# Performance work log

Measured on AMD Instinct MI355X. Metric: run time of the kernel, lower is better.

The kernel has to match this reference:

```python
import jax, jax.numpy as jnp
import numpy as np

N = 4096       # number of graph nodes
F_IN = 512     # in_features == out_features (residual connection requires it)
H = 8          # n_heads


def setup_inputs() -> dict:
    key = jax.random.key(0)
    k1, k2, k3, k4, k5 = jax.random.split(key, 5)
    s = 1.0 / np.sqrt(F_IN)  # keep projections well-scaled
    x = jax.random.normal(k1, (N, F_IN), dtype=jnp.float32)
    Wq = jax.random.normal(k2, (F_IN, F_IN), dtype=jnp.float32) * s
    Wk = jax.random.normal(k3, (F_IN, F_IN), dtype=jnp.float32) * s
    Wv = jax.random.normal(k4, (F_IN, F_IN), dtype=jnp.float32) * s
    adj = jax.random.randint(k5, (H, N, N), 0, 2, dtype=jnp.int32)
    return {"x": x, "Wq": Wq, "Wk": Wk, "Wv": Wv, "adj": adj}


def reference(x, Wq, Wk, Wv, adj):
    # Faithful to torch GraphAttentionLayer.forward (eval mode, dropout off).
    # NOTE: the torch code builds keys = input.repeat(N,1,1).detach() -> the
    # K/V inputs are stop-gradient copies of x; projections are per-node, so
    # we compute them once instead of materializing the redundant [N,N,F].
    n, f = x.shape
    d = f // H  # head dim (chunk_size)
    xk = jax.lax.stop_gradient(x)
    # nn.Linear: y = x @ W.T ; split feature dim into heads -> [H, N, d]
    Q = (x @ Wq.T).reshape(n, H, d).transpose(1, 0, 2)
    K = (xk @ Wk.T).reshape(n, H, d).transpose(1, 0, 2)
    V = (xk @ Wv.T).reshape(n, H, d).transpose(1, 0, 2)
    # scaled by sqrt(in_features) (NOT head dim), as in the original
    scores = jnp.einsum('hnd,hmd->hnm', Q, K) / jnp.sqrt(jnp.float32(f))
    scores = jnp.where(adj > 0, scores, jnp.float32(-9e15))
    attn = jax.nn.softmax(scores, axis=-1)          # [H, N, N]
    out = jnp.einsum('hnm,hmd->hnd', attn, V)       # [H, N, d]
    out = out.transpose(1, 0, 2).reshape(n, f)      # concat heads -> [N, F]
    return jax.nn.elu(out + x)[:, None, :]          # [N, 1, F] like torch
```

## Files before the change

### kernel.cpp

```cpp
#include <hip/hip_runtime.h>
#include <hip/hip_bf16.h>

#define NN 4096
#define FF 512
#define NH 8
#define DH 64

typedef __attribute__((ext_vector_type(8))) short bf16x8;
typedef __attribute__((ext_vector_type(4))) float f32x4;

#define X_OFF  0
#define W_OFF  2097152
#define QF_OFF 2883584
#define KF_OFF 4980736
#define VF_OFF 7077888
#define PACC_OFF 9175040
#define PDEN_USHORT_OFF 17563648
#define PK_USHORT_OFF 17825792

__device__ __forceinline__ ushort f2bf(float f) {
    __hip_bfloat16 h = __float2bfloat16(f);
    return __builtin_bit_cast(ushort, h);
}
__device__ __forceinline__ float bf2f(ushort u) {
    unsigned int v = ((unsigned int)u) << 16;
    return __builtin_bit_cast(float, v);
}

__global__ __launch_bounds__(256) void cvt_kernel(const float* __restrict__ x,
                                                  const float* __restrict__ wq,
                                                  const float* __restrict__ wk,
                                                  const float* __restrict__ wv,
                                                  ushort* __restrict__ ws) {
    int i = blockIdx.x * 256 + threadIdx.x;
    int base = i * 4;
    const float* src;
    int off;
    float sc = 1.f;
    if (base < 2097152) { src = x; off = base; }
    else {
        int t = base - 2097152;
        int m = t >> 18;
        src = (m == 0) ? wq : ((m == 1) ? wk : wv);
        if (m == 0) sc = 0.044194173824159216f;
        off = t & 262143;
    }
    float4 v = *reinterpret_cast<const float4*>(src + off);
    ushort4 o;
    o.x = f2bf(v.x * sc); o.y = f2bf(v.y * sc); o.z = f2bf(v.z * sc); o.w = f2bf(v.w * sc);
    *reinterpret_cast<ushort4*>(ws + base) = o;
}

__global__ __launch_bounds__(256) void packqkv_kernel(const int* __restrict__ adj,
                                                      unsigned int* __restrict__ pk,
                                                      ushort* __restrict__ ws) {
    int bid = blockIdx.x;
    int wave = threadIdx.x >> 6, lane = threadIdx.x & 63;

    if (bid < 8192) {
        int row = bid * 4 + wave;
        const int* ar = adj + (size_t)row * 4096;
        unsigned long long* outp = reinterpret_cast<unsigned long long*>(pk + (size_t)row * 128);
        for (int it = 0; it < 64; it += 4) {
            int v0 = __builtin_nontemporal_load(ar + (it + 0) * 64 + lane);
            int v1 = __builtin_nontemporal_load(ar + (it + 1) * 64 + lane);
            int v2 = __builtin_nontemporal_load(ar + (it + 2) * 64 + lane);
            int v3 = __builtin_nontemporal_load(ar + (it + 3) * 64 + lane);
            unsigned long long b0 = __ballot(v0 != 0);
            unsigned long long b1 = __ballot(v1 != 0);
            unsigned long long b2 = __ballot(v2 != 0);
            unsigned long long b3 = __ballot(v3 != 0);
            if (lane == 0) {
                outp[it + 0] = b0;
                outp[it + 1] = b1;
                outp[it + 2] = b2;
                outp[it + 3] = b3;
            }
        }
        return;
    }

    int q = bid - 8192;
    int mat = q >> 9;
    int rem = q & 511;
    int fb = rem & 7;
    int mb = rem >> 3;
    int la = lane & 15, lk = lane >> 4;

    int m_base = mb * 64 + wave * 16;
    int f_base = fb * 64;

    const ushort* xb = ws + X_OFF;
    const ushort* wb = ws + W_OFF + mat * 262144;

    f32x4 acc[4];
#pragma unroll
    for (int t = 0; t < 4; ++t) acc[t] = (f32x4){0.f, 0.f, 0.f, 0.f};

#pragma unroll 4
    for (int k0 = 0; k0 < 512; k0 += 32) {
        bf16x8 a = *reinterpret_cast<const bf16x8*>(xb + (size_t)(m_base + la) * 512 + k0 + lk * 8);
#pragma unroll
        for (int ft = 0; ft < 4; ++ft) {
            bf16x8 b = *reinterpret_cast<const bf16x8*>(wb + (size_t)(f_base + ft * 16 + la) * 512 + k0 + lk * 8);
            acc[ft] = __builtin_amdgcn_mfma_f32_16x16x32_bf16(a, b, acc[ft], 0, 0, 0);
        }
    }

#pragma unroll
    for (int ft = 0; ft < 4; ++ft) {
#pragma unroll
        for (int r = 0; r < 4; ++r) {
            int n = m_base + lk * 4 + r;
            int d = ft * 16 + la;
            ushort v = f2bf(acc[ft][r]);
            if (mat < 2) {
                ushort* base = ws + (mat == 0 ? QF_OFF : KF_OFF) + (size_t)fb * 262144;
                int blk = n >> 4, rr = n & 15;
                int half = d >> 5, lkk = (d >> 3) & 3, e = d & 7;
                base[(((size_t)blk * 2 + half) * 64 + lkk * 16 + rr) * 8 + e] = v;
            } else {
                ushort* base = ws + VF_OFF + (size_t)fb * 262144;
                int kb64 = n >> 6, kc = n & 63;
                int hf = kc >> 5, lkv = (kc >> 3) & 3, ev = kc & 7;
                int dt = d >> 4, lav = d & 15;
                base[((((size_t)kb64 * 4 + dt) * 2 + hf) * 64 + lkv * 16 + lav) * 8 + ev] = v;
            }
        }
    }
}

__global__ __launch_bounds__(256, 3) void attn_kernel(const unsigned int* __restrict__ pk,
                                                      const ushort* __restrict__ ws,
                                                      ushort* __restrict__ pacc,
                                                      float* __restrict__ pden) {
    __shared__ ushort kbuf[2][8][512];
    __shared__ ushort vbuf[2][8][512];
    __shared__ ushort P[4][16][72];

    int bid = blockIdx.x;
    int h = bid & 7, qb = (bid >> 3) & 63, ks = bid >> 9;
    int wave = threadIdx.x >> 6, lane = threadIdx.x & 63;
    int la = lane & 15, lk = lane >> 4;
    int q0w = qb * 64 + wave * 16;
    int lk4 = lk * 4;

    const ushort* Qh = ws + QF_OFF + (size_t)h * 262144;
    const ushort* Kh = ws + KF_OFF + (size_t)h * 262144;
    const ushort* Vh = ws + VF_OFF + (size_t)h * 262144;
    const unsigned int* mrow = pk + ((size_t)h * 4096 + q0w + la) * 128;

    bf16x8 qa0 = *reinterpret_cast<const bf16x8*>(Qh + ((((size_t)(q0w >> 4)) * 2 + 0) * 64 + lane) * 8);
    bf16x8 qa1 = *reinterpret_cast<const bf16x8*>(Qh + ((((size_t)(q0w >> 4)) * 2 + 1) * 64 + lane) * 8);

    f32x4 acc[4];
#pragma unroll
    for (int r = 0; r < 4; ++r) acc[r] = (f32x4){0.f, 0.f, 0.f, 0.f};
    float den = 0.f;

    const f32x4 zero = {0.f, 0.f, 0.f, 0.f};
    int kb0 = ks * 16;

#define STAGE(BUF, KB)                                                                     \
    {                                                                                      \
        const ushort* sbase_ = (wave < 2) ? Kh : Vh;                                       \
        ushort(*dbuf_)[512] = (wave < 2) ? kbuf[BUF] : vbuf[BUF];                          \
        int t0_ = (wave & 1) * 4;                                                          \
        _Pragma("unroll")                                                                  \
        for (int t_ = 0; t_ < 4; ++t_) {                                                   \
            int tile_ = t0_ + t_;                                                          \
            const ushort* src_ = sbase_ +                                                  \
                (((size_t)(KB) * 4 + (tile_ >> 1)) * 2 + (tile_ & 1)) * 512 + lane * 8;    \
            __builtin_amdgcn_global_load_lds(                                              \
                (const __attribute__((address_space(1))) unsigned int*)src_,               \
                (__attribute__((address_space(3))) unsigned int*)&dbuf_[tile_][0],         \
                16, 0, 0);                                                                 \
        }                                                                                  \
    }

    STAGE(0, kb0)

    for (int it = 0; it < 16; ++it) {
        int kb = kb0 + it;
        int cur = it & 1;

        asm volatile("s_waitcnt vmcnt(0)" ::: "memory");
        __builtin_amdgcn_s_barrier();

        if (it < 15) STAGE(cur ^ 1, kb + 1)

        uint2 mk = *reinterpret_cast<const uint2*>(mrow + kb * 2);

#pragma unroll
        for (int kt = 0; kt < 4; ++kt) {
            bf16x8 kf0 = *reinterpret_cast<const bf16x8*>(&kbuf[cur][kt * 2 + 0][lane * 8]);
            bf16x8 kf1 = *reinterpret_cast<const bf16x8*>(&kbuf[cur][kt * 2 + 1][lane * 8]);
            f32x4 s = __builtin_amdgcn_mfma_f32_16x16x32_bf16(kf0, qa0, zero, 0, 0, 0);
            s = __builtin_amdgcn_mfma_f32_16x16x32_bf16(kf1, qa1, s, 0, 0, 0);
            unsigned int dw = (kt < 2) ? mk.x : mk.y;
            int sh = ((kt & 1) << 4) + lk4;
            ushort4 pw;
            float e0 = __expf(((dw >> (sh + 0)) & 1u) ? s[0] : -1e30f);
            float e1 = __expf(((dw >> (sh + 1)) & 1u) ? s[1] : -1e30f);
            float e2 = __expf(((dw >> (sh + 2)) & 1u) ? s[2] : -1e30f);
            float e3 = __expf(((dw >> (sh + 3)) & 1u) ? s[3] : -1e30f);
            den += (e0 + e1) + (e2 + e3);
            pw.x = f2bf(e0); pw.y = f2bf(e1); pw.z = f2bf(e2); pw.w = f2bf(e3);
            *reinterpret_cast<ushort4*>(&P[wave][la][kt * 16 + lk4]) = pw;
        }

        bf16x8 pa0 = *reinterpret_cast<const bf16x8*>(&P[wave][la][lk * 8]);
        bf16x8 pa1 = *reinterpret_cast<const bf16x8*>(&P[wave][la][32 + lk * 8]);
#pragma unroll
        for (int dt = 0; dt < 4; ++dt) {
            bf16x8 vb0 = *reinterpret_cast<const bf16x8*>(&vbuf[cur][dt * 2 + 0][lane * 8]);
            bf16x8 vb1 = *reinterpret_cast<const bf16x8*>(&vbuf[cur][dt * 2 + 1][lane * 8]);
            acc[dt] = __builtin_amdgcn_mfma_f32_16x16x32_bf16(pa0, vb0, acc[dt], 0, 0, 0);
            acc[dt] = __builtin_amdgcn_mfma_f32_16x16x32_bf16(pa1, vb1, acc[dt], 0, 0, 0);
        }
    }

    den += __shfl_xor(den, 16, 64);
    den += __shfl_xor(den, 32, 64);

    ushort* pa_out = pacc + ((size_t)ks * 8 + h) * 4096 * 64;
#pragma unroll
    for (int dt = 0; dt < 4; ++dt)
#pragma unroll
        for (int r = 0; r < 4; ++r) {
            int qi = q0w + lk4 + r;
            __builtin_nontemporal_store(f2bf(acc[dt][r]), pa_out + (size_t)qi * 64 + dt * 16 + la);
        }
    if (lane < 16) {
        float* pd = pden + ((size_t)ks * 8 + h) * 4096;
        pd[q0w + lane] = den;
    }
#undef STAGE
}

__global__ __launch_bounds__(256) void combine_kernel(const float* __restrict__ x,
                                                      const ushort* __restrict__ pacc,
                                                      const float* __restrict__ pden,
                                                      float* __restrict__ out) {
    int idx = blockIdx.x * 256 + threadIdx.x;
    int n = idx >> 7, fq = idx & 127;
    int h = fq >> 4;
    int d4 = (fq & 15) * 4;

    float4 o = make_float4(0.f, 0.f, 0.f, 0.f);
    float den = 0.f;
#pragma unroll
    for (int ksp = 0; ksp < 4; ++ksp) {
        const ushort* pa = pacc + (((size_t)ksp * 8 + h) * 4096 + n) * 64 + d4;
        ushort4 p = *reinterpret_cast<const ushort4*>(pa);
        o.x += bf2f(p.x); o.y += bf2f(p.y); o.z += bf2f(p.z); o.w += bf2f(p.w);
        den += pden[((size_t)ksp * 8 + h) * 4096 + n];
    }
    float4 xv = *reinterpret_cast<const float4*>(x + (size_t)n * 512 + fq * 4);
    float inv = 1.f / den;
    float4 r;
    r.x = o.x * inv + xv.x;
    r.y = o.y * inv + xv.y;
    r.z = o.z * inv + xv.z;
    r.w = o.w * inv + xv.w;
    r.x = (r.x > 0.f) ? r.x : (__expf(r.x) - 1.f);
    r.y = (r.y > 0.f) ? r.y : (__expf(r.y) - 1.f);
    r.z = (r.z > 0.f) ? r.z : (__expf(r.z) - 1.f);
    r.w = (r.w > 0.f) ? r.w : (__expf(r.w) - 1.f);
    *reinterpret_cast<float4*>(out + (size_t)n * 512 + fq * 4) = r;
}

extern "C" void kernel_launch(void* const* d_in, const int* in_sizes, int n_in,
                              void* d_out, int out_size, void* d_ws, size_t ws_size,
                              hipStream_t stream) {
    const float* x  = (const float*)d_in[0];
    const float* wq = (const float*)d_in[1];
    const float* wk = (const float*)d_in[2];
    const float* wv = (const float*)d_in[3];
    const int*   adj = (const int*)d_in[4];
    float* out = (float*)d_out;
    ushort* ws = (ushort*)d_ws;
    ushort* pacc = ws + PACC_OFF;
    float* pden = (float*)(ws + PDEN_USHORT_OFF);
    unsigned int* pk = (unsigned int*)(ws + PK_USHORT_OFF);

    cvt_kernel<<<2816, 256, 0, stream>>>(x, wq, wk, wv, ws);
    packqkv_kernel<<<9728, 256, 0, stream>>>(adj, pk, ws);
    attn_kernel<<<2048, 256, 0, stream>>>(pk, ws, pacc, pden);
    combine_kernel<<<2048, 256, 0, stream>>>(x, pacc, pden, out);
}
```

Baseline: 226.8 us.

## Process two query tiles per wave and split keys three ways

Each wave now handles 32 query rows instead of 16, so every K/V tile staged in LDS is reused across twice as many queries. The key dimension is split into 3 uneven chunks (22/21/21 blocks) instead of 4, which cuts the grid to 768 blocks and the partial-sum traffic read by the combine kernel. The aim is less LDS staging and global K/V traffic per unit of work. In exchange, register pressure rises and far fewer blocks are in flight, which may reduce occupancy and latency hiding on the GPU.

```diff
diff --git a/kernel.cpp b/kernel.cpp
--- a/kernel.cpp
+++ b/kernel.cpp
@@ -136,30 +136,39 @@
                                                       float* __restrict__ pden) {
     __shared__ ushort kbuf[2][8][512];
     __shared__ ushort vbuf[2][8][512];
-    __shared__ ushort P[4][16][72];
+    __shared__ ushort P[4][2][16][72];
 
     int bid = blockIdx.x;
-    int h = bid & 7, qb = (bid >> 3) & 63, ks = bid >> 9;
+    int h = bid & 7, qb = (bid >> 3) & 31, ks = bid >> 8;
     int wave = threadIdx.x >> 6, lane = threadIdx.x & 63;
     int la = lane & 15, lk = lane >> 4;
-    int q0w = qb * 64 + wave * 16;
+    int q0w = qb * 128 + wave * 32;
     int lk4 = lk * 4;
 
     const ushort* Qh = ws + QF_OFF + (size_t)h * 262144;
     const ushort* Kh = ws + KF_OFF + (size_t)h * 262144;
     const ushort* Vh = ws + VF_OFF + (size_t)h * 262144;
-    const unsigned int* mrow = pk + ((size_t)h * 4096 + q0w + la) * 128;
-
-    bf16x8 qa0 = *reinterpret_cast<const bf16x8*>(Qh + ((((size_t)(q0w >> 4)) * 2 + 0) * 64 + lane) * 8);
-    bf16x8 qa1 = *reinterpret_cast<const bf16x8*>(Qh + ((((size_t)(q0w >> 4)) * 2 + 1) * 64 + lane) * 8);
-
-    f32x4 acc[4];
-#pragma unroll
-    for (int r = 0; r < 4; ++r) acc[r] = (f32x4){0.f, 0.f, 0.f, 0.f};
-    float den = 0.f;
+    const unsigned int* mrow0 = pk + ((size_t)h * 4096 + q0w + la) * 128;
+    const unsigned int* mrow1 = mrow0 + 16 * 128;
+
+    bf16x8 qa[2][2];
+#pragma unroll
+    for (int qs = 0; qs < 2; ++qs)
+#pragma unroll
+        for (int hf = 0; hf < 2; ++hf)
+            qa[qs][hf] = *reinterpret_cast<const bf16x8*>(
+                Qh + ((((size_t)((q0w >> 4) + qs)) * 2 + hf) * 64 + lane) * 8);
+
+    f32x4 acc[2][4];
+    float den[2] = {0.f, 0.f};
+#pragma unroll
+    for (int qs = 0; qs < 2; ++qs)
+#pragma unroll
+        for (int r = 0; r < 4; ++r) acc[qs][r] = (f32x4){0.f, 0.f, 0.f, 0.f};
 
     const f32x4 zero = {0.f, 0.f, 0.f, 0.f};
-    int kb0 = ks * 16;
+    int kb_begin = ks * 21 + (ks ? 1 : 0);
+    int kb_count = 22 - (ks ? 1 : 0);
 
 #define STAGE(BUF, KB)                                                                     \
     {                                                                                      \
@@ -178,62 +187,78 @@
         }                                                                                  \
     }
 
-    STAGE(0, kb0)
-
-    for (int it = 0; it < 16; ++it) {
-        int kb = kb0 + it;
+    STAGE(0, kb_begin)
+
+    for (int it = 0; it < kb_count; ++it) {
+        int kb = kb_begin + it;
         int cur = it & 1;
 
         asm volatile("s_waitcnt vmcnt(0)" ::: "memory");
         __builtin_amdgcn_s_barrier();
 
-        if (it < 15) STAGE(cur ^ 1, kb + 1)
-
-        uint2 mk = *reinterpret_cast<const uint2*>(mrow + kb * 2);
+        if (it + 1 < kb_count) STAGE(cur ^ 1, kb + 1)
+
+        uint2 mk0 = *reinterpret_cast<const uint2*>(mrow0 + kb * 2);
+        uint2 mk1 = *reinterpret_cast<const uint2*>(mrow1 + kb * 2);
 
 #pragma unroll
         for (int kt = 0; kt < 4; ++kt) {
             bf16x8 kf0 = *reinterpret_cast<const bf16x8*>(&kbuf[cur][kt * 2 + 0][lane * 8]);
             bf16x8 kf1 = *reinterpret_cast<const bf16x8*>(&kbuf[cur][kt * 2 + 1][lane * 8]);
-            f32x4 s = __builtin_amdgcn_mfma_f32_16x16x32_bf16(kf0, qa0, zero, 0, 0, 0);
-            s = __builtin_amdgcn_mfma_f32_16x16x32_bf16(kf1, qa1, s, 0, 0, 0);
-            unsigned int dw = (kt < 2) ? mk.x : mk.y;
             int sh = ((kt & 1) << 4) + lk4;
-            ushort4 pw;
-            float e0 = __expf(((dw >> (sh + 0)) & 1u) ? s[0] : -1e30f);
-            float e1 = __expf(((dw >> (sh + 1)) & 1u) ? s[1] : -1e30f);
-            float e2 = __expf(((dw >> (sh + 2)) & 1u) ? s[2] : -1e30f);
-            float e3 = __expf(((dw >> (sh + 3)) & 1u) ? s[3] : -1e30f);
-            den += (e0 + e1) + (e2 + e3);
-            pw.x = f2bf(e0); pw.y = f2bf(e1); pw.z = f2bf(e2); pw.w = f2bf(e3);
-            *reinterpret_cast<ushort4*>(&P[wave][la][kt * 16 + lk4]) = pw;
-        }
-
-        bf16x8 pa0 = *reinterpret_cast<const bf16x8*>(&P[wave][la][lk * 8]);
-        bf16x8 pa1 = *reinterpret_cast<const bf16x8*>(&P[wave][la][32 + lk * 8]);
+#pragma unroll
+            for (int qs = 0; qs < 2; ++qs) {
+                f32x4 s = __builtin_amdgcn_mfma_f32_16x16x32_bf16(kf0, qa[qs][0], zero, 0, 0, 0);
+                s = __builtin_amdgcn_mfma_f32_16x16x32_bf16(kf1, qa[qs][1], s, 0, 0, 0);
+                unsigned int dw = qs ? ((kt < 2) ? mk1.x : mk1.y) : ((kt < 2) ? mk0.x : mk0.y);
+                ushort4 pw;
+                float e0 = __expf(((dw >> (sh + 0)) & 1u) ? s[0] : -1e30f);
+                float e1 = __expf(((dw >> (sh + 1)) & 1u) ? s[1] : -1e30f);
+                float e2 = __expf(((dw >> (sh + 2)) & 1u) ? s[2] : -1e30f);
+                float e3 = __expf(((dw >> (sh + 3)) & 1u) ? s[3] : -1e30f);
+                den[qs] += (e0 + e1) + (e2 + e3);
+                pw.x = f2bf(e0); pw.y = f2bf(e1); pw.z = f2bf(e2); pw.w = f2bf(e3);
+                *reinterpret_cast<ushort4*>(&P[wave][qs][la][kt * 16 + lk4]) = pw;
+            }
+        }
+
+        bf16x8 pa[2][2];
+#pragma unroll
+        for (int qs = 0; qs < 2; ++qs) {
+            pa[qs][0] = *reinterpret_cast<const bf16x8*>(&P[wave][qs][la][lk * 8]);
+            pa[qs][1] = *reinterpret_cast<const bf16x8*>(&P[wave][qs][la][32 + lk * 8]);
+        }
 #pragma unroll
         for (int dt = 0; dt < 4; ++dt) {
             bf16x8 vb0 = *reinterpret_cast<const bf16x8*>(&vbuf[cur][dt * 2 + 0][lane * 8]);
             bf16x8 vb1 = *reinterpret_cast<const bf16x8*>(&vbuf[cur][dt * 2 + 1][lane * 8]);
-            acc[dt] = __builtin_amdgcn_mfma_f32_16x16x32_bf16(pa0, vb0, acc[dt], 0, 0, 0);
-            acc[dt] = __builtin_amdgcn_mfma_f32_16x16x32_bf16(pa1, vb1, acc[dt], 0, 0, 0);
-        }
-    }
-
-    den += __shfl_xor(den, 16, 64);
-    den += __shfl_xor(den, 32, 64);
+            acc[0][dt] = __builtin_amdgcn_mfma_f32_16x16x32_bf16(pa[0][0], vb0, acc[0][dt], 0, 0, 0);
+            acc[0][dt] = __builtin_amdgcn_mfma_f32_16x16x32_bf16(pa[0][1], vb1, acc[0][dt], 0, 0, 0);
+            acc[1][dt] = __builtin_amdgcn_mfma_f32_16x16x32_bf16(pa[1][0], vb0, acc[1][dt], 0, 0, 0);
+            acc[1][dt] = __builtin_amdgcn_mfma_f32_16x16x32_bf16(pa[1][1], vb1, acc[1][dt], 0, 0, 0);
+        }
+    }
+
+#pragma unroll
+    for (int qs = 0; qs < 2; ++qs) {
+        den[qs] += __shfl_xor(den[qs], 16, 64);
+        den[qs] += __shfl_xor(den[qs], 32, 64);
+    }
 
     ushort* pa_out = pacc + ((size_t)ks * 8 + h) * 4096 * 64;
 #pragma unroll
-    for (int dt = 0; dt < 4; ++dt)
-#pragma unroll
-        for (int r = 0; r < 4; ++r) {
-            int qi = q0w + lk4 + r;
-            __builtin_nontemporal_store(f2bf(acc[dt][r]), pa_out + (size_t)qi * 64 + dt * 16 + la);
-        }
+    for (int qs = 0; qs < 2; ++qs)
+#pragma unroll
+        for (int dt = 0; dt < 4; ++dt)
+#pragma unroll
+            for (int r = 0; r < 4; ++r) {
+                int qi = q0w + qs * 16 + lk4 + r;
+                __builtin_nontemporal_store(f2bf(acc[qs][dt][r]), pa_out + (size_t)qi * 64 + dt * 16 + la);
+            }
     if (lane < 16) {
         float* pd = pden + ((size_t)ks * 8 + h) * 4096;
-        pd[q0w + lane] = den;
+        pd[q0w + lane] = den[0];
+        pd[q0w + 16 + lane] = den[1];
     }
 #undef STAGE
 }
@@ -250,7 +275,7 @@
     float4 o = make_float4(0.f, 0.f, 0.f, 0.f);
     float den = 0.f;
 #pragma unroll
-    for (int ksp = 0; ksp < 4; ++ksp) {
+    for (int ksp = 0; ksp < 3; ++ksp) {
         const ushort* pa = pacc + (((size_t)ksp * 8 + h) * 4096 + n) * 64 + d4;
         ushort4 p = *reinterpret_cast<const ushort4*>(pa);
         o.x += bf2f(p.x); o.y += bf2f(p.y); o.z += bf2f(p.z); o.w += bf2f(p.w);
@@ -286,6 +311,6 @@
 
     cvt_kernel<<<2816, 256, 0, stream>>>(x, wq, wk, wv, ws);
     packqkv_kernel<<<9728, 256, 0, stream>>>(adj, pk, ws);
-    attn_kernel<<<2048, 256, 0, stream>>>(pk, ws, pacc, pden);
+    attn_kernel<<<768, 256, 0, stream>>>(pk, ws, pacc, pden);
     combine_kernel<<<2048, 256, 0, stream>>>(x, pacc, pden, out);
 }
```

New measurement: 218.1 us. -3.9%, faster.
